# Kernel optimization log

Hardware: AMD Instinct MI355X
Metric: run time of the kernel (lower is better)

The kernel has to match this reference:

```python
import jax, jax.numpy as jnp
import numpy as np

B, T, DIM, H = 4, 2048, 1024, 16
HD = DIM // H  # 64
ROPE_BASE = 10000.0


def _rope_cos_sin(seq_len, head_dim, dtype):
    # lucidrains rotary-embedding-torch convention: interleaved pairs.
    inv_freq = 1.0 / (ROPE_BASE ** (jnp.arange(0, head_dim, 2, dtype=jnp.float32) / head_dim))
    freqs = jnp.arange(seq_len, dtype=jnp.float32)[:, None] * inv_freq[None, :]  # [T, hd/2]
    freqs = jnp.repeat(freqs, 2, axis=-1)  # [T, hd], each freq duplicated for the pair
    return jnp.cos(freqs).astype(dtype), jnp.sin(freqs).astype(dtype)


def _rotate_half(x):
    # interleaved pairs: (x1, x2) -> (-x2, x1)
    x = x.reshape(*x.shape[:-1], -1, 2)
    x1, x2 = x[..., 0], x[..., 1]
    return jnp.stack([-x2, x1], axis=-1).reshape(*x.shape[:-2], -1)


def _apply_rope(x, cos, sin):
    # x: [B, H, T, hd]; cos/sin: [T, hd]
    return x * cos[None, None, :, :] + _rotate_half(x) * sin[None, None, :, :]


def setup_inputs() -> dict:
    key = jax.random.key(0)
    kx, kqkv, kw, kb = jax.random.split(key, 4)
    s_qkv = 1.0 / np.sqrt(DIM)
    return {
        "x": jax.random.normal(kx, (B, T, DIM), dtype=jnp.float32),
        "w_qkv": jax.random.normal(kqkv, (3 * DIM, DIM), dtype=jnp.float32) * s_qkv,
        "w_proj": jax.random.normal(kw, (DIM, DIM), dtype=jnp.float32) * s_qkv,
        "b_proj": jax.random.normal(kb, (DIM,), dtype=jnp.float32) * 0.01,
    }


def reference(x, w_qkv, w_proj, b_proj):
    b, t, c = x.shape
    qkv = jnp.einsum('btc,dc->btd', x, w_qkv)  # [B, T, 3*C]
    qkv = qkv.reshape(b, t, 3, H, HD).transpose(2, 0, 3, 1, 4)  # [3, B, H, T, hd]
    q, k, v = qkv[0], qkv[1], qkv[2]

    cos, sin = _rope_cos_sin(t, HD, x.dtype)
    q = _apply_rope(q, cos, sin)
    k = _apply_rope(k, cos, sin)

    scale = 1.0 / np.sqrt(HD)
    scores = jnp.einsum('bhqd,bhkd->bhqk', q, k) * scale  # [B, H, T, T]
    attn = jax.nn.softmax(scores, axis=-1)
    out = jnp.einsum('bhqk,bhkd->bhqd', attn, v)  # [B, H, T, hd]

    out = out.transpose(0, 2, 1, 3).reshape(b, t, c)  # [B, T, C]
    return jnp.einsum('btc,dc->btd', out, w_proj) + b_proj
```

## Files before the change

### kernel.cpp

```cpp
#include <hip/hip_runtime.h>
#include <hip/hip_bf16.h>
#include <math.h>

#define Bz   4
#define Tz   2048
#define DIMz 1024
#define Hz   16
#define HDz  64
#define BHz  (Bz*Hz)
#define Mz   (Bz*Tz)
#define LOG2E 1.44269504088896340736f
#define QSCALE (0.125f * LOG2E)

typedef __attribute__((ext_vector_type(8))) __bf16 bf16x8;
typedef __attribute__((ext_vector_type(4))) __bf16 bf16x4;
typedef __attribute__((ext_vector_type(4))) float  f32x4;

__device__ __forceinline__ f32x4 mfma_16x16x32(bf16x8 a, bf16x8 b, f32x4 c) {
  return __builtin_amdgcn_mfma_f32_16x16x32_bf16(a, b, c, 0, 0, 0);
}

__device__ __forceinline__ ushort f2bf(float f) {
  unsigned u = __float_as_uint(f);
  u += 0x7fffu + ((u >> 16) & 1u);
  return (ushort)(u >> 16);
}
__device__ __forceinline__ float bf2f(ushort h) {
  return __uint_as_float(((unsigned)h) << 16);
}

__device__ __forceinline__ void gl_lds16(const ushort* g, ushort* l) {
  __builtin_amdgcn_global_load_lds(
      (const __attribute__((address_space(1))) unsigned int*)g,
      (__attribute__((address_space(3))) unsigned int*)l, 16, 0, 0);
}

__global__ void k_cvt(const float4* __restrict__ in, ushort4* __restrict__ out, int n4) {
  int i = blockIdx.x * blockDim.x + threadIdx.x;
  if (i >= n4) return;
  float4 v = in[i];
  ushort4 o;
  o.x = f2bf(v.x); o.y = f2bf(v.y); o.z = f2bf(v.z); o.w = f2bf(v.w);
  out[i] = o;
}

__global__ void k_rope_tab(float* __restrict__ tab) {
  int idx = blockIdx.x * blockDim.x + threadIdx.x;
  if (idx >= Tz * 32) return;
  int t = idx >> 5, i = idx & 31;
  double ang = (double)t * exp(((double)(-2 * i) / (double)HDz) * log(10000.0));
  tab[2 * idx]     = (float)cos(ang);
  tab[2 * idx + 1] = (float)sin(ang);
}


__global__ __launch_bounds__(256) void k_gemm_qkv(const ushort* __restrict__ A,
                                                  const ushort* __restrict__ Bw,
                                                  ushort* __restrict__ qb,
                                                  ushort* __restrict__ kb,
                                                  ushort* __restrict__ vbt) {
  __shared__ ushort As[128 * 64];
  __shared__ ushort Bs[128 * 64];
  const int tid = threadIdx.x;
  const int bm = (blockIdx.x & 63) << 7;
  const int bn = (blockIdx.x >> 6) << 7;
  const int wid = tid >> 6, lane = tid & 63;
  const int wr = (wid & 1) << 6, wc = (wid >> 1) << 6;
  const int lr = lane & 15, lg = lane >> 4;

  const int r8 = lane >> 3;
  const int cswz = (((lane & 7) ^ r8) << 3);
  const ushort* pA = A  + (size_t)(bm + wid * 8 + r8) * 1024 + cswz;
  const ushort* pB = Bw + (size_t)(bn + wid * 8 + r8) * 1024 + cswz;
  ushort* lA = &As[wid * 512];
  ushort* lB = &Bs[wid * 512];

  const int cs0 = ((lg ^ (lr & 7)) << 3);
  const int cs1 = cs0 ^ 32;

  const f32x4 fz = {0.f, 0.f, 0.f, 0.f};
  f32x4 acc[4][4];
  #pragma unroll
  for (int i = 0; i < 4; i++)
    #pragma unroll
    for (int j = 0; j < 4; j++) acc[i][j] = fz;

  for (int k0 = 0; k0 < 1024; k0 += 64) {
    __syncthreads();
    #pragma unroll
    for (int rep = 0; rep < 4; rep++) {
      gl_lds16(pA + (size_t)rep * 32768 + k0, lA + rep * 2048);
      gl_lds16(pB + (size_t)rep * 32768 + k0, lB + rep * 2048);
    }
    __syncthreads();
    #pragma unroll
    for (int kc = 0; kc < 2; kc++) {
      const int cs = kc ? cs1 : cs0;
      bf16x8 af[4], bfr[4];
      #pragma unroll
      for (int i = 0; i < 4; i++)
        af[i] = *reinterpret_cast<const bf16x8*>(&As[(wr + i * 16 + lr) * 64 + cs]);
      #pragma unroll
      for (int j = 0; j < 4; j++)
        bfr[j] = *reinterpret_cast<const bf16x8*>(&Bs[(wc + j * 16 + lr) * 64 + cs]);
      #pragma unroll
      for (int i = 0; i < 4; i++)
        #pragma unroll
        for (int j = 0; j < 4; j++)
          acc[i][j] = mfma_16x16x32(af[i], bfr[j], acc[i][j]);
    }
  }

  #pragma unroll
  for (int j = 0; j < 4; j++) {
    int col = bn + wc + j * 16 + lr;
    int which = col >> 10;
    int r = col & 1023;
    int h = r >> 6, hd = r & 63;
    #pragma unroll
    for (int i = 0; i < 4; i++) {
      int row0 = bm + wr + i * 16 + lg * 4;
      int b = row0 >> 11, t0 = row0 & 2047;
      if (which == 2) {
        uint lo = (uint)f2bf(acc[i][j][0]) | ((uint)f2bf(acc[i][j][1]) << 16);
        uint hi = (uint)f2bf(acc[i][j][2]) | ((uint)f2bf(acc[i][j][3]) << 16);
        *reinterpret_cast<uint2*>(&vbt[((size_t)(b * Hz + h) * HDz + hd) * Tz + t0]) =
            make_uint2(lo, hi);
      } else {
        ushort* dst = (which == 0) ? qb : kb;
        #pragma unroll
        for (int q = 0; q < 4; q++)
          dst[(((size_t)(b * Hz + h) * Tz + t0 + q) << 6) + hd] = f2bf(acc[i][j][q]);
      }
    }
  }
}

__global__ void k_rope(ushort* __restrict__ qb, ushort* __restrict__ kb,
                       const float* __restrict__ tab) {
  int idx = blockIdx.x * blockDim.x + threadIdx.x;
  const int per = BHz * Tz * 8;
  if (idx >= 2 * per) return;
  bool isq = (idx < per);
  ushort* base = isq ? qb : kb;
  float sc = isq ? QSCALE : 1.0f;
  int j = isq ? idx : idx - per;
  int g = j & 7;
  int t = (j >> 3) & (Tz - 1);
  int bh = j >> 14;
  ushort* p = base + ((size_t)bh * Tz + t) * 64 + g * 8;
  const float* tb = tab + ((size_t)t * 32 + g * 4) * 2;
  float4 c0 = *reinterpret_cast<const float4*>(tb);
  float4 c1 = *reinterpret_cast<const float4*>(tb + 4);
  union { uint4 v; ushort s[8]; } u;
  u.v = *reinterpret_cast<const uint4*>(p);
  float e[8];
  #pragma unroll
  for (int e_i = 0; e_i < 8; e_i++) e[e_i] = bf2f(u.s[e_i]);
  float cs[8] = {c0.x, c0.y, c0.z, c0.w, c1.x, c1.y, c1.z, c1.w};
  #pragma unroll
  for (int m = 0; m < 4; m++) {
    float c = cs[2 * m], s = cs[2 * m + 1];
    float x1 = e[2 * m], x2 = e[2 * m + 1];
    u.s[2 * m]     = f2bf((x1 * c - x2 * s) * sc);
    u.s[2 * m + 1] = f2bf((x2 * c + x1 * s) * sc);
  }
  *reinterpret_cast<uint4*>(p) = u.v;
}

__global__ __launch_bounds__(256) void k_attn(const ushort* __restrict__ qb,
                                              const ushort* __restrict__ kb,
                                              const ushort* __restrict__ vbt,
                                              ushort* __restrict__ ao) {
  __shared__ ushort Ks[2][64 * 64];
  __shared__ ushort Vs[2][64 * 64];
  __shared__ ushort Ps[4][32 * 64];

  const int bid = ((blockIdx.x & 7) << 7) + (blockIdx.x >> 3);
  const int qt = bid & 15;
  const int bh = bid >> 4;
  const int tid = threadIdx.x, wid = tid >> 6, lane = tid & 63;
  const int lr = lane & 15, lg = lane >> 4;

  const ushort* Qg = qb + ((size_t)bh * Tz + qt * 128 + wid * 32) * HDz;
  const ushort* Kg = kb + (size_t)bh * Tz * HDz;
  const ushort* Vg = vbt + (size_t)bh * HDz * Tz;

  bf16x8 qA0 = *reinterpret_cast<const bf16x8*>(&Qg[lr * 64 + lg * 8]);
  bf16x8 qA1 = *reinterpret_cast<const bf16x8*>(&Qg[lr * 64 + lg * 8 + 32]);
  bf16x8 qB0 = *reinterpret_cast<const bf16x8*>(&Qg[(16 + lr) * 64 + lg * 8]);
  bf16x8 qB1 = *reinterpret_cast<const bf16x8*>(&Qg[(16 + lr) * 64 + lg * 8 + 32]);

  bf16x8 onev;
  #pragma unroll
  for (int j = 0; j < 8; j++) onev[j] = (__bf16)1.0f;

  const int r8 = lane >> 3;
  const int cswz = (((lane & 7) ^ r8) << 3);
  const ushort* kb0 = Kg + (size_t)(wid * 16 + r8) * 64 + cswz;
  const ushort* kb1 = kb0 + 8 * 64;
  const ushort* vb0 = Vg + (size_t)(wid * 16 + r8) * Tz + cswz;
  const ushort* vb1 = vb0 + (size_t)8 * Tz;

  const f32x4 fz = {0.f, 0.f, 0.f, 0.f};
  f32x4 oaccA[4], oaccB[4];
  #pragma unroll
  for (int db = 0; db < 4; db++) { oaccA[db] = fz; oaccB[db] = fz; }
  f32x4 laccA = fz, laccB = fz;

  const int cs0 = ((lg ^ (lr & 7)) << 3);
  const int cs1 = cs0 ^ 32;
  const int swz8 = (lr & 7) << 3;

  {
    ushort* kl = &Ks[0][wid * 1024];
    ushort* vl = &Vs[0][wid * 1024];
    gl_lds16(kb0, kl); gl_lds16(kb1, kl + 512);
    gl_lds16(vb0, vl); gl_lds16(vb1, vl + 512);
  }
  __syncthreads();

  int cur = 0;
  for (int kt = 0; kt < Tz / 64; kt++) {
    if (kt + 1 < Tz / 64) {
      ushort* kl = &Ks[cur ^ 1][wid * 1024];
      ushort* vl = &Vs[cur ^ 1][wid * 1024];
      gl_lds16(kb0 + (size_t)(kt + 1) * 4096, kl);
      gl_lds16(kb1 + (size_t)(kt + 1) * 4096, kl + 512);
      gl_lds16(vb0 + (kt + 1) * 64, vl);
      gl_lds16(vb1 + (kt + 1) * 64, vl + 512);
    }

    f32x4 stA[4], stB[4];
    #pragma unroll
    for (int nb = 0; nb < 4; nb++) {
      const ushort* kp = &Ks[cur][(nb * 16 + lr) * 64];
      bf16x8 kf0 = *reinterpret_cast<const bf16x8*>(kp + cs0);
      bf16x8 kf1 = *reinterpret_cast<const bf16x8*>(kp + cs1);
      stA[nb] = mfma_16x16x32(kf0, qA0, fz);
      stA[nb] = mfma_16x16x32(kf1, qA1, stA[nb]);
      stB[nb] = mfma_16x16x32(kf0, qB0, fz);
      stB[nb] = mfma_16x16x32(kf1, qB1, stB[nb]);
    }

    #pragma unroll
    for (int nb = 0; nb < 4; nb++) {
      bf16x4 pa, pb;
      #pragma unroll
      for (int r = 0; r < 4; r++) {
        pa[r] = (__bf16)__builtin_exp2f(stA[nb][r]);
        pb[r] = (__bf16)__builtin_exp2f(stB[nb][r]);
      }
      const int c = (16 * nb + 4 * lg) ^ swz8;
      *reinterpret_cast<bf16x4*>(&Ps[wid][lr * 64 + c]) = pa;
      *reinterpret_cast<bf16x4*>(&Ps[wid][(16 + lr) * 64 + c]) = pb;
    }
    asm volatile("s_waitcnt lgkmcnt(0)" ::: "memory");
    const ushort* ppA = &Ps[wid][lr * 64];
    const ushort* ppB = &Ps[wid][(16 + lr) * 64];
    bf16x8 pfA0 = *reinterpret_cast<const bf16x8*>(ppA + cs0);
    bf16x8 pfA1 = *reinterpret_cast<const bf16x8*>(ppA + cs1);
    bf16x8 pfB0 = *reinterpret_cast<const bf16x8*>(ppB + cs0);
    bf16x8 pfB1 = *reinterpret_cast<const bf16x8*>(ppB + cs1);

    laccA = mfma_16x16x32(pfA0, onev, laccA);
    laccA = mfma_16x16x32(pfA1, onev, laccA);
    laccB = mfma_16x16x32(pfB0, onev, laccB);
    laccB = mfma_16x16x32(pfB1, onev, laccB);

    #pragma unroll
    for (int db = 0; db < 4; db++) {
      const ushort* vp = &Vs[cur][(db * 16 + lr) * 64];
      bf16x8 vf0 = *reinterpret_cast<const bf16x8*>(vp + cs0);
      bf16x8 vf1 = *reinterpret_cast<const bf16x8*>(vp + cs1);
      oaccA[db] = mfma_16x16x32(pfA0, vf0, oaccA[db]);
      oaccA[db] = mfma_16x16x32(pfA1, vf1, oaccA[db]);
      oaccB[db] = mfma_16x16x32(pfB0, vf0, oaccB[db]);
      oaccB[db] = mfma_16x16x32(pfB1, vf1, oaccB[db]);
    }

    __syncthreads();
    cur ^= 1;
  }

  const int b = bh >> 4, h = bh & 15;
  #pragma unroll
  for (int r = 0; r < 4; r++) {
    float invA = 1.0f / laccA[r];
    float invB = 1.0f / laccB[r];
    int tA = qt * 128 + wid * 32 + lg * 4 + r;
    size_t baseA = ((size_t)(b * Tz + tA) * Hz + h) * HDz;
    size_t baseB = ((size_t)(b * Tz + tA + 16) * Hz + h) * HDz;
    #pragma unroll
    for (int db = 0; db < 4; db++) {
      ao[baseA + db * 16 + lr] = f2bf(oaccA[db][r] * invA);
      ao[baseB + db * 16 + lr] = f2bf(oaccB[db][r] * invB);
    }
  }
}

__global__ __launch_bounds__(256) void k_gemm_proj(const ushort* __restrict__ A,
                                                   const ushort* __restrict__ Bw,
                                                   const float* __restrict__ bias,
                                                   float* __restrict__ out) {
  __shared__ ushort As[128 * 64];
  __shared__ ushort Bs[128 * 64];
  const int tid = threadIdx.x;
  const int bm = (blockIdx.x & 63) << 7;
  const int bn = (blockIdx.x >> 6) << 7;
  const int wid = tid >> 6, lane = tid & 63;
  const int wr = (wid & 1) << 6, wc = (wid >> 1) << 6;
  const int lr = lane & 15, lg = lane >> 4;

  const int r8 = lane >> 3;
  const int cswz = (((lane & 7) ^ r8) << 3);
  const ushort* pA = A  + (size_t)(bm + wid * 8 + r8) * 1024 + cswz;
  const ushort* pB = Bw + (size_t)(bn + wid * 8 + r8) * 1024 + cswz;
  ushort* lA = &As[wid * 512];
  ushort* lB = &Bs[wid * 512];

  const int cs0 = ((lg ^ (lr & 7)) << 3);
  const int cs1 = cs0 ^ 32;

  const f32x4 fz = {0.f, 0.f, 0.f, 0.f};
  f32x4 acc[4][4];
  #pragma unroll
  for (int i = 0; i < 4; i++)
    #pragma unroll
    for (int j = 0; j < 4; j++) acc[i][j] = fz;

  for (int k0 = 0; k0 < 1024; k0 += 64) {
    __syncthreads();
    #pragma unroll
    for (int rep = 0; rep < 4; rep++) {
      gl_lds16(pA + (size_t)rep * 32768 + k0, lA + rep * 2048);
      gl_lds16(pB + (size_t)rep * 32768 + k0, lB + rep * 2048);
    }
    __syncthreads();
    #pragma unroll
    for (int kc = 0; kc < 2; kc++) {
      const int cs = kc ? cs1 : cs0;
      bf16x8 af[4], bfr[4];
      #pragma unroll
      for (int i = 0; i < 4; i++)
        af[i] = *reinterpret_cast<const bf16x8*>(&As[(wr + i * 16 + lr) * 64 + cs]);
      #pragma unroll
      for (int j = 0; j < 4; j++)
        bfr[j] = *reinterpret_cast<const bf16x8*>(&Bs[(wc + j * 16 + lr) * 64 + cs]);
      #pragma unroll
      for (int i = 0; i < 4; i++)
        #pragma unroll
        for (int j = 0; j < 4; j++)
          acc[i][j] = mfma_16x16x32(af[i], bfr[j], acc[i][j]);
    }
  }

  #pragma unroll
  for (int j = 0; j < 4; j++) {
    int col = bn + wc + j * 16 + lr;
    float bv = bias[col];
    #pragma unroll
    for (int i = 0; i < 4; i++) {
      #pragma unroll
      for (int q = 0; q < 4; q++) {
        int row = bm + wr + i * 16 + lg * 4 + q;
        out[(size_t)row * 1024 + col] = acc[i][j][q] + bv;
      }
    }
  }
}

extern "C" void kernel_launch(void* const* d_in, const int* in_sizes, int n_in,
                              void* d_out, int out_size, void* d_ws, size_t ws_size,
                              hipStream_t stream) {
  const float* x      = (const float*)d_in[0];
  const float* w_qkv  = (const float*)d_in[1];
  const float* w_proj = (const float*)d_in[2];
  const float* b_proj = (const float*)d_in[3];
  float* out = (float*)d_out;

  char* ws = (char*)d_ws;
  ushort* xh     = (ushort*)ws; ws += (size_t)Mz * DIMz * 2;
  ushort* wqkvh  = (ushort*)ws; ws += (size_t)3 * DIMz * DIMz * 2;
  ushort* wprojh = (ushort*)ws; ws += (size_t)DIMz * DIMz * 2;
  ushort* qbuf   = (ushort*)ws; ws += (size_t)BHz * Tz * HDz * 2;
  ushort* kbuf   = (ushort*)ws; ws += (size_t)BHz * Tz * HDz * 2;
  ushort* vbuft  = (ushort*)ws; ws += (size_t)BHz * HDz * Tz * 2;
  ushort* aout   = (ushort*)ws; ws += (size_t)Mz * DIMz * 2;
  float*  tab    = (float*)ws;  ws += (size_t)Tz * 32 * 2 * 4;

  k_cvt<<<8192, 256, 0, stream>>>((const float4*)x,      (ushort4*)xh,     Mz * DIMz / 4);
  k_cvt<<<3072, 256, 0, stream>>>((const float4*)w_qkv,  (ushort4*)wqkvh,  3 * DIMz * DIMz / 4);
  k_cvt<<<1024, 256, 0, stream>>>((const float4*)w_proj, (ushort4*)wprojh, DIMz * DIMz / 4);
  k_rope_tab<<<256, 256, 0, stream>>>(tab);
  k_gemm_qkv<<<64 * 24, 256, 0, stream>>>(xh, wqkvh, qbuf, kbuf, vbuft);
  k_rope<<<8192, 256, 0, stream>>>(qbuf, kbuf, tab);
  k_attn<<<BHz * (Tz / 128), 256, 0, stream>>>(qbuf, kbuf, vbuft, aout);
  k_gemm_proj<<<64 * 8, 256, 0, stream>>>(aout, wprojh, b_proj, out);
}
```

Baseline: 230.8 us.

## Fuse RoPE into QKV GEMM epilogue and halve attention P scratch

```diff
diff --git a/kernel.cpp b/kernel.cpp
--- a/kernel.cpp
+++ b/kernel.cpp
@@ -56,6 +56,7 @@
 
 __global__ __launch_bounds__(256) void k_gemm_qkv(const ushort* __restrict__ A,
                                                   const ushort* __restrict__ Bw,
+                                                  const float* __restrict__ tab,
                                                   ushort* __restrict__ qb,
                                                   ushort* __restrict__ kb,
                                                   ushort* __restrict__ vbt) {
@@ -128,53 +129,29 @@
             make_uint2(lo, hi);
       } else {
         ushort* dst = (which == 0) ? qb : kb;
+        const float sc = (which == 0) ? QSCALE : 1.0f;
+        const float sgn = (hd & 1) ? 1.0f : -1.0f;
+        const float* tb = &tab[((size_t)t0 * 32 + (hd >> 1)) * 2];
         #pragma unroll
-        for (int q = 0; q < 4; q++)
-          dst[(((size_t)(b * Hz + h) * Tz + t0 + q) << 6) + hd] = f2bf(acc[i][j][q]);
+        for (int q = 0; q < 4; q++) {
+          float own = acc[i][j][q];
+          float other = __shfl_xor(own, 1);
+          float c = tb[q * 64], s = tb[q * 64 + 1];
+          dst[(((size_t)(b * Hz + h) * Tz + t0 + q) << 6) + hd] =
+              f2bf((own * c + sgn * other * s) * sc);
+        }
       }
     }
   }
 }
 
-__global__ void k_rope(ushort* __restrict__ qb, ushort* __restrict__ kb,
-                       const float* __restrict__ tab) {
-  int idx = blockIdx.x * blockDim.x + threadIdx.x;
-  const int per = BHz * Tz * 8;
-  if (idx >= 2 * per) return;
-  bool isq = (idx < per);
-  ushort* base = isq ? qb : kb;
-  float sc = isq ? QSCALE : 1.0f;
-  int j = isq ? idx : idx - per;
-  int g = j & 7;
-  int t = (j >> 3) & (Tz - 1);
-  int bh = j >> 14;
-  ushort* p = base + ((size_t)bh * Tz + t) * 64 + g * 8;
-  const float* tb = tab + ((size_t)t * 32 + g * 4) * 2;
-  float4 c0 = *reinterpret_cast<const float4*>(tb);
-  float4 c1 = *reinterpret_cast<const float4*>(tb + 4);
-  union { uint4 v; ushort s[8]; } u;
-  u.v = *reinterpret_cast<const uint4*>(p);
-  float e[8];
-  #pragma unroll
-  for (int e_i = 0; e_i < 8; e_i++) e[e_i] = bf2f(u.s[e_i]);
-  float cs[8] = {c0.x, c0.y, c0.z, c0.w, c1.x, c1.y, c1.z, c1.w};
-  #pragma unroll
-  for (int m = 0; m < 4; m++) {
-    float c = cs[2 * m], s = cs[2 * m + 1];
-    float x1 = e[2 * m], x2 = e[2 * m + 1];
-    u.s[2 * m]     = f2bf((x1 * c - x2 * s) * sc);
-    u.s[2 * m + 1] = f2bf((x2 * c + x1 * s) * sc);
-  }
-  *reinterpret_cast<uint4*>(p) = u.v;
-}
-
-__global__ __launch_bounds__(256) void k_attn(const ushort* __restrict__ qb,
-                                              const ushort* __restrict__ kb,
-                                              const ushort* __restrict__ vbt,
-                                              ushort* __restrict__ ao) {
+__global__ __launch_bounds__(256, 4) void k_attn(const ushort* __restrict__ qb,
+                                                 const ushort* __restrict__ kb,
+                                                 const ushort* __restrict__ vbt,
+                                                 ushort* __restrict__ ao) {
   __shared__ ushort Ks[2][64 * 64];
   __shared__ ushort Vs[2][64 * 64];
-  __shared__ ushort Ps[4][32 * 64];
+  __shared__ ushort Ps[4][16 * 64];
 
   const int bid = ((blockIdx.x & 7) << 7) + (blockIdx.x >> 3);
   const int qt = bid & 15;
@@ -232,6 +209,7 @@
     }
 
     f32x4 stA[4], stB[4];
+    __builtin_amdgcn_s_setprio(1);
     #pragma unroll
     for (int nb = 0; nb < 4; nb++) {
       const ushort* kp = &Ks[cur][(nb * 16 + lr) * 64];
@@ -242,32 +220,38 @@
       stB[nb] = mfma_16x16x32(kf0, qB0, fz);
       stB[nb] = mfma_16x16x32(kf1, qB1, stB[nb]);
     }
-
+    __builtin_amdgcn_s_setprio(0);
+
+    bf16x4 pa[4], pbv[4];
     #pragma unroll
     for (int nb = 0; nb < 4; nb++) {
-      bf16x4 pa, pb;
       #pragma unroll
       for (int r = 0; r < 4; r++) {
-        pa[r] = (__bf16)__builtin_exp2f(stA[nb][r]);
-        pb[r] = (__bf16)__builtin_exp2f(stB[nb][r]);
+        pa[nb][r]  = (__bf16)__builtin_exp2f(stA[nb][r]);
+        pbv[nb][r] = (__bf16)__builtin_exp2f(stB[nb][r]);
       }
-      const int c = (16 * nb + 4 * lg) ^ swz8;
-      *reinterpret_cast<bf16x4*>(&Ps[wid][lr * 64 + c]) = pa;
-      *reinterpret_cast<bf16x4*>(&Ps[wid][(16 + lr) * 64 + c]) = pb;
-    }
+    }
+
+    #pragma unroll
+    for (int nb = 0; nb < 4; nb++)
+      *reinterpret_cast<bf16x4*>(&Ps[wid][lr * 64 + ((16 * nb + 4 * lg) ^ swz8)]) = pa[nb];
     asm volatile("s_waitcnt lgkmcnt(0)" ::: "memory");
-    const ushort* ppA = &Ps[wid][lr * 64];
-    const ushort* ppB = &Ps[wid][(16 + lr) * 64];
-    bf16x8 pfA0 = *reinterpret_cast<const bf16x8*>(ppA + cs0);
-    bf16x8 pfA1 = *reinterpret_cast<const bf16x8*>(ppA + cs1);
-    bf16x8 pfB0 = *reinterpret_cast<const bf16x8*>(ppB + cs0);
-    bf16x8 pfB1 = *reinterpret_cast<const bf16x8*>(ppB + cs1);
-
+    const ushort* pp = &Ps[wid][lr * 64];
+    bf16x8 pfA0 = *reinterpret_cast<const bf16x8*>(pp + cs0);
+    bf16x8 pfA1 = *reinterpret_cast<const bf16x8*>(pp + cs1);
+
+    #pragma unroll
+    for (int nb = 0; nb < 4; nb++)
+      *reinterpret_cast<bf16x4*>(&Ps[wid][lr * 64 + ((16 * nb + 4 * lg) ^ swz8)]) = pbv[nb];
+    asm volatile("s_waitcnt lgkmcnt(0)" ::: "memory");
+    bf16x8 pfB0 = *reinterpret_cast<const bf16x8*>(pp + cs0);
+    bf16x8 pfB1 = *reinterpret_cast<const bf16x8*>(pp + cs1);
+
+    __builtin_amdgcn_s_setprio(1);
     laccA = mfma_16x16x32(pfA0, onev, laccA);
     laccA = mfma_16x16x32(pfA1, onev, laccA);
     laccB = mfma_16x16x32(pfB0, onev, laccB);
     laccB = mfma_16x16x32(pfB1, onev, laccB);
-
     #pragma unroll
     for (int db = 0; db < 4; db++) {
       const ushort* vp = &Vs[cur][(db * 16 + lr) * 64];
@@ -278,6 +262,7 @@
       oaccB[db] = mfma_16x16x32(pfB0, vf0, oaccB[db]);
       oaccB[db] = mfma_16x16x32(pfB1, vf1, oaccB[db]);
     }
+    __builtin_amdgcn_s_setprio(0);
 
     __syncthreads();
     cur ^= 1;
@@ -393,8 +378,7 @@
   k_cvt<<<3072, 256, 0, stream>>>((const float4*)w_qkv,  (ushort4*)wqkvh,  3 * DIMz * DIMz / 4);
   k_cvt<<<1024, 256, 0, stream>>>((const float4*)w_proj, (ushort4*)wprojh, DIMz * DIMz / 4);
   k_rope_tab<<<256, 256, 0, stream>>>(tab);
-  k_gemm_qkv<<<64 * 24, 256, 0, stream>>>(xh, wqkvh, qbuf, kbuf, vbuft);
-  k_rope<<<8192, 256, 0, stream>>>(qbuf, kbuf, tab);
+  k_gemm_qkv<<<64 * 24, 256, 0, stream>>>(xh, wqkvh, tab, qbuf, kbuf, vbuft);
   k_attn<<<BHz * (Tz / 128), 256, 0, stream>>>(qbuf, kbuf, vbuft, aout);
   k_gemm_proj<<<64 * 8, 256, 0, stream>>>(aout, wprojh, b_proj, out);
 }
```

Result: faster. 215.0 us (-6.9%).
